# Kernel tuning notes

Measured on AMD Instinct MI355X. Metric: run time of the kernel, lower is better.

## Reference

```python
import jax, jax.numpy as jnp
import numpy as np

B, D_IN = 8192, 4096
H1, H2, LAT = 2048, 1024, 256
NQ, NL = 16, 2


def setup_inputs() -> dict:
    key = jax.random.key(0)
    ks = jax.random.split(key, 16)
    def lin(k, fan_in, fan_out):
        k1, k2 = jax.random.split(k)
        s = 1.0 / np.sqrt(fan_in)
        W = jax.random.uniform(k1, (fan_out, fan_in), jnp.float32, -s, s)
        b = jax.random.uniform(k2, (fan_out,), jnp.float32, -s, s)
        return W, b
    x = jax.random.normal(ks[0], (B, D_IN), jnp.float32)
    We1, be1 = lin(ks[1], D_IN, H1)
    We2, be2 = lin(ks[2], H1, H2)
    We3, be3 = lin(ks[3], H2, LAT)
    P = jax.random.normal(ks[4], (NL, NQ, 3), jnp.float32)  # ansatz params (rx,ry,rz)
    Wd1, bd1 = lin(ks[5], NQ, H2)
    Wd2, bd2 = lin(ks[6], H2, H1)
    Wd3, bd3 = lin(ks[7], H1, D_IN)
    return {"x": x, "We1": We1, "be1": be1, "We2": We2, "be2": be2,
            "We3": We3, "be3": be3, "P": P, "Wd1": Wd1, "bd1": bd1,
            "Wd2": Wd2, "bd2": bd2, "Wd3": Wd3, "bd3": bd3}


def _quantum_block(latent, P):
    """Exact simulation of the per-qubit circuit (all gates single-qubit, so the
    2^n statevector factorizes into per-qubit 2-vectors (a,b) over |0>,|1>).
    latent: (B, LAT), P: (NL, NQ, 3). Returns Z-expectations (B, NQ)."""
    nq = P.shape[1]
    th = latent[:, :nq]  # encoding RY angles, (B, NQ)
    # RY(th)|0> = cos(th/2)|0> + sin(th/2)|1>
    a = jnp.cos(th / 2).astype(jnp.complex64)  # (B, NQ)
    b = jnp.sin(th / 2).astype(jnp.complex64)
    for l in range(P.shape[0]):
        # RX
        t = P[l, :, 0] / 2
        c, s = jnp.cos(t).astype(jnp.complex64), jnp.sin(t).astype(jnp.complex64)
        a, b = c * a - 1j * s * b, -1j * s * a + c * b
        # RY
        t = P[l, :, 1] / 2
        c, s = jnp.cos(t).astype(jnp.complex64), jnp.sin(t).astype(jnp.complex64)
        a, b = c * a - s * b, s * a + c * b
        # RZ
        t = P[l, :, 2] / 2
        ph = jnp.exp(-1j * t.astype(jnp.complex64))
        a, b = a * ph, b * jnp.conj(ph)
    z = (a.real ** 2 + a.imag ** 2) - (b.real ** 2 + b.imag ** 2)
    return z.astype(latent.dtype)


def reference(x, We1, be1, We2, be2, We3, be3, P,
              Wd1, bd1, Wd2, bd2, Wd3, bd3):
    h = jax.nn.relu(x @ We1.T + be1)
    h = jax.nn.relu(h @ We2.T + be2)
    latent = h @ We3.T + be3            # (B, LAT)
    refined = _quantum_block(latent, P)  # (B, NQ)
    h = jax.nn.relu(refined @ Wd1.T + bd1)
    h = jax.nn.relu(h @ Wd2.T + bd2)
    return h @ Wd3.T + bd3              # (B, D_IN)
```

## Files before the change

kernel.cpp:

```cpp
#include <hip/hip_runtime.h>

typedef __attribute__((ext_vector_type(8))) short bf16x8;
typedef __attribute__((ext_vector_type(4))) float f32x4;

__device__ __forceinline__ unsigned short f2bf(float f) {
    union { float f; unsigned int u; } v; v.f = f;
    unsigned int u = v.u;
    unsigned int r = (u + 0x7FFFu + ((u >> 16) & 1u)) >> 16;
    return (unsigned short)r;
}
__device__ __forceinline__ float bf2f(unsigned short b) {
    union { unsigned int u; float f; } v; v.u = ((unsigned int)b) << 16;
    return v.f;
}

#define GL16(g, l)                                                             \
    __builtin_amdgcn_global_load_lds(                                          \
        (__attribute__((address_space(1))) void*)(void*)(g),                   \
        (__attribute__((address_space(3))) void*)(void*)(l), 16, 0, 0)

#define SBAR() __builtin_amdgcn_sched_barrier(0)
#define BAR()  do { SBAR(); __builtin_amdgcn_s_barrier(); SBAR(); } while (0)

struct Cast5 {
    const float *s0, *s1, *s2, *s3, *s4;
    unsigned short *d0, *d1, *d2, *d3, *d4;
    int n0, n1, n2, n3, total;
};
__global__ void castall(Cast5 a) {
    int stride = gridDim.x * blockDim.x;
    for (int i = blockIdx.x * blockDim.x + threadIdx.x; i < a.total; i += stride) {
        int j = i; const float* s; unsigned short* d;
        if (j < a.n0) { s = a.s0; d = a.d0; }
        else { j -= a.n0;
            if (j < a.n1) { s = a.s1; d = a.d1; }
            else { j -= a.n1;
                if (j < a.n2) { s = a.s2; d = a.d2; }
                else { j -= a.n2;
                    if (j < a.n3) { s = a.s3; d = a.d3; }
                    else { j -= a.n3; s = a.s4; d = a.d4; } } } }
        float4 v = ((const float4*)s)[j];
        ushort4 o;
        o.x = f2bf(v.x); o.y = f2bf(v.y); o.z = f2bf(v.z); o.w = f2bf(v.w);
        ((ushort4*)d)[j] = o;
    }
}


template<int RELU, int OUT_BF16, int MP>
__global__ __launch_bounds__(512, 2) void gemm8p(
    const unsigned short* __restrict__ A,
    const unsigned short* __restrict__ Bm,
    const float* __restrict__ bias,
    void* __restrict__ Cout,
    int N, int K, int NT)
{
    constexpr int AHU  = MP * 2048;
    constexpr int BOFF = MP * 8192;
    __shared__ __align__(16) unsigned short lds[MP * 8192 + 32768];

    const int tid  = threadIdx.x;
    const int lane = tid & 63;
    const int w    = tid >> 6;
    const int wm   = w >> 2;
    const int wn   = w & 3;
    const int bm   = blockIdx.y;
    const int bn   = blockIdx.x;

    const long arow0 = (long)bm * (MP * 64);
    const long brow0 = (long)bn * 256;

    const int sc0 = tid,      sc1 = 512 + tid;
    const int sr0 = sc0 >> 3, sr1 = sc1 >> 3;
    const int so0 = (((sc0 & 7) * 16) ^ ((sr0 & 7) << 4)) >> 1;
    const int so1 = (((sc1 & 7) * 16) ^ ((sr1 & 7) << 4)) >> 1;
    const int soff0 = sr0 * K + so0;
    const int soff1 = sr1 * K + so1;
    const int lb0 = (w * 64) * 8;
    const int lb1 = (512 + w * 64) * 8;

    const int cl  = lane & 15;
    const int g16 = (lane >> 4) * 16;
    const int sw  = (cl & 7) << 4;
    const int cK0 = (g16 ^ sw) >> 1;
    const int cK1 = ((64 + g16) ^ sw) >> 1;
    const int arb = wm * (MP * 16) + cl;
    const int brb = wn * 32 + cl;

    f32x4  acc[2][2][MP][2] = {};
    bf16x8 a0[MP][2], a1[MP][2], b0[2][2], b1[2][2];

#define STAGE_A(t2, h) do {                                                    \
        int b_  = (t2) & 1;                                                    \
        int tt_ = (t2) >= NT ? (t2) - NT : (t2);                               \
        const unsigned short* gb_ = A + (arow0 + (long)(h) * (MP * 32)) * (long)K + (long)tt_ * 64; \
        unsigned short* lh_ = &lds[(b_ * 2 + (h)) * AHU];                      \
        GL16(gb_ + soff0, lh_ + lb0);                                          \
        if constexpr (MP == 4) { GL16(gb_ + soff1, lh_ + lb1); }               \
    } while (0)
#define STAGE_B(t2, h) do {                                                    \
        int b_  = (t2) & 1;                                                    \
        int tt_ = (t2) >= NT ? (t2) - NT : (t2);                               \
        const unsigned short* gb_ = Bm + (brow0 + (long)(h) * 128) * (long)K + (long)tt_ * 64; \
        unsigned short* lh_ = &lds[BOFF + (b_ * 2 + (h)) * 8192];              \
        GL16(gb_ + soff0, lh_ + lb0);                                          \
        GL16(gb_ + soff1, lh_ + lb1);                                          \
    } while (0)

#define READA(AR, mh, b_) do {                                                 \
        const unsigned short* ab_ = &lds[((b_) * 2 + (mh)) * AHU];             \
        _Pragma("unroll") for (int mp_ = 0; mp_ < MP; ++mp_) {                 \
            const unsigned short* rp_ = ab_ + (arb + mp_ * 16) * 64;           \
            AR[mp_][0] = *(const bf16x8*)(rp_ + cK0);                          \
            AR[mp_][1] = *(const bf16x8*)(rp_ + cK1);                          \
        }                                                                      \
    } while (0)
#define READB(BR, nh, b_) do {                                                 \
        const unsigned short* bb_ = &lds[BOFF + ((b_) * 2 + (nh)) * 8192];     \
        _Pragma("unroll") for (int np_ = 0; np_ < 2; ++np_) {                  \
            const unsigned short* rp_ = bb_ + (brb + np_ * 16) * 64;           \
            BR[np_][0] = *(const bf16x8*)(rp_ + cK0);                          \
            BR[np_][1] = *(const bf16x8*)(rp_ + cK1);                          \
        }                                                                      \
    } while (0)
#define QUAD(mh, nh, AR, BR) do {                                              \
        __builtin_amdgcn_s_setprio(1);                                         \
        _Pragma("unroll") for (int kk_ = 0; kk_ < 2; ++kk_)                    \
        _Pragma("unroll") for (int mp_ = 0; mp_ < MP; ++mp_)                   \
        _Pragma("unroll") for (int np_ = 0; np_ < 2; ++np_)                    \
            acc[mh][nh][mp_][np_] = __builtin_amdgcn_mfma_f32_16x16x32_bf16(   \
                AR[mp_][kk_], BR[np_][kk_], acc[mh][nh][mp_][np_], 0, 0, 0);   \
        __builtin_amdgcn_s_setprio(0);                                         \
    } while (0)
#define VMW() do {                                                             \
        SBAR();                                                                \
        if constexpr (MP == 4) asm volatile("s_waitcnt vmcnt(6)" ::: "memory");\
        else                   asm volatile("s_waitcnt vmcnt(5)" ::: "memory");\
        SBAR();                                                                \
    } while (0)

    STAGE_B(0, 0); STAGE_A(0, 0); STAGE_B(0, 1); STAGE_A(0, 1);
    STAGE_B(1, 0); STAGE_A(1, 0); STAGE_B(1, 1);
    VMW();
    BAR();
    READA(a0, 0, 0);
    READB(b0, 0, 0);

    for (int t = 0; t < NT; ++t) {
        const int b = t & 1;
        READA(a1, 1, b);
        STAGE_A(t + 1, 1);
        BAR();
        QUAD(0, 0, a0, b0);
        BAR();
        READB(b1, 1, b);
        STAGE_B(t + 2, 0);
        VMW();
        BAR();
        QUAD(0, 1, a0, b1);
        BAR();
        READA(a0, 0, b ^ 1);
        STAGE_A(t + 2, 0);
        BAR();
        QUAD(1, 1, a1, b1);
        BAR();
        STAGE_B(t + 2, 1);
        VMW();
        BAR();
        QUAD(1, 0, a1, b0);
        READB(b0, 0, b ^ 1);
        BAR();
    }

    SBAR(); asm volatile("s_waitcnt vmcnt(0)" ::: "memory"); SBAR();
    BAR();

    const int r4 = (lane >> 4) * 4;
    float bv[2][2];
    #pragma unroll
    for (int nh = 0; nh < 2; ++nh)
        #pragma unroll
        for (int np = 0; np < 2; ++np)
            bv[nh][np] = bias[(long)bn * 256 + nh * 128 + wn * 32 + np * 16 + cl];

    if (OUT_BF16) {
        unsigned short* epi = lds;
        #pragma unroll
        for (int h = 0; h < 2; ++h) {
            if (h) BAR();
            #pragma unroll
            for (int mp = 0; mp < MP; ++mp)
                #pragma unroll
                for (int nh = 0; nh < 2; ++nh)
                    #pragma unroll
                    for (int np = 0; np < 2; ++np)
                        #pragma unroll
                        for (int r = 0; r < 4; ++r) {
                            float v = acc[h][nh][mp][np][r] + bv[nh][np];
                            if (RELU) v = fmaxf(v, 0.f);
                            int lrow = wm * (MP * 16) + mp * 16 + r4 + r;
                            int lcol = nh * 128 + wn * 32 + np * 16 + cl;
                            epi[lrow * 264 + lcol] = f2bf(v);
                        }
            BAR();
            long rowg0 = (long)bm * (MP * 64) + h * (MP * 32);
            #pragma unroll
            for (int i = 0; i < 2 * MP; ++i) {
                int row = (tid >> 5) + i * 16;
                int cc  = (tid & 31) * 8;
                bf16x8 v8 = *(const bf16x8*)&epi[row * 264 + cc];
                *(bf16x8*)((unsigned short*)Cout + (rowg0 + row) * (long)N + (long)bn * 256 + cc) = v8;
            }
        }
    } else {
        #pragma unroll
        for (int mh = 0; mh < 2; ++mh)
            #pragma unroll
            for (int mp = 0; mp < MP; ++mp) {
                long grow = (long)bm * (MP * 64) + mh * (MP * 32) + wm * (MP * 16) + mp * 16 + r4;
                #pragma unroll
                for (int nh = 0; nh < 2; ++nh)
                    #pragma unroll
                    for (int np = 0; np < 2; ++np) {
                        long gcol = (long)bn * 256 + nh * 128 + wn * 32 + np * 16 + cl;
                        #pragma unroll
                        for (int r = 0; r < 4; ++r) {
                            float v = acc[mh][nh][mp][np][r] + bv[nh][np];
                            if (RELU) v = fmaxf(v, 0.f);
                            ((float*)Cout)[(grow + r) * (long)N + gcol] = v;
                        }
                    }
            }
    }
#undef STAGE_A
#undef STAGE_B
#undef READA
#undef READB
#undef QUAD
#undef VMW
}

__global__ __launch_bounds__(256) void latq_d1(
    const unsigned short* __restrict__ h2,
    const float* __restrict__ We3,
    const float* __restrict__ be3,
    const float* __restrict__ P,
    const float* __restrict__ Wd1,
    const float* __restrict__ bd1,
    unsigned short* __restrict__ h3)
{
    __shared__ float zsh[4][16];
    const int lane = threadIdx.x & 63;
    const int wv   = threadIdx.x >> 6;
    const long row = (long)blockIdx.x * 4 + wv;

    float hreg[16];
    const unsigned short* hr = h2 + row * 1024;
    #pragma unroll
    for (int j = 0; j < 16; ++j) hreg[j] = bf2f(hr[lane + 64 * j]);

    float myth = 0.f;
    #pragma unroll
    for (int q = 0; q < 16; ++q) {
        const float* wq = We3 + q * 1024;
        float p = 0.f;
        #pragma unroll
        for (int j = 0; j < 16; ++j) p += hreg[j] * wq[lane + 64 * j];
        #pragma unroll
        for (int o = 32; o; o >>= 1) p += __shfl_xor(p, o, 64);
        if (lane == q) myth = p + be3[q];
    }

    if (lane < 16) {
        const int q = lane;
        float ar = cosf(0.5f * myth), ai = 0.f;
        float br = sinf(0.5f * myth), bi = 0.f;
        #pragma unroll
        for (int l = 0; l < 2; ++l) {
            const float* pp = P + (l * 16 + q) * 3;
            float t, c, s, ar2, ai2, br2, bi2;
            t = 0.5f * pp[0]; c = cosf(t); s = sinf(t);
            ar2 = c * ar + s * bi;  ai2 = c * ai - s * br;
            br2 = c * br + s * ai;  bi2 = c * bi - s * ar;
            ar = ar2; ai = ai2; br = br2; bi = bi2;
            t = 0.5f * pp[1]; c = cosf(t); s = sinf(t);
            ar2 = c * ar - s * br;  ai2 = c * ai - s * bi;
            br2 = s * ar + c * br;  bi2 = s * ai + c * bi;
            ar = ar2; ai = ai2; br = br2; bi = bi2;
            t = 0.5f * pp[2]; c = cosf(t); s = sinf(t);
            ar2 = ar * c + ai * s;  ai2 = ai * c - ar * s;
            br2 = br * c - bi * s;  bi2 = bi * c + br * s;
            ar = ar2; ai = ai2; br = br2; bi = bi2;
        }
        zsh[wv][q] = ar * ar + ai * ai - (br * br + bi * bi);
    }
    __syncthreads();

    float z[16];
    #pragma unroll
    for (int q = 0; q < 16; ++q) z[q] = zsh[wv][q];

    unsigned short* orow = h3 + row * 1024;
    #pragma unroll
    for (int i = 0; i < 16; ++i) {
        int j = lane + 64 * i;
        const float4* wrow = (const float4*)(Wd1 + j * 16);
        float acc = bd1[j];
        #pragma unroll
        for (int qq = 0; qq < 4; ++qq) {
            float4 w4 = wrow[qq];
            acc += z[qq * 4 + 0] * w4.x + z[qq * 4 + 1] * w4.y
                 + z[qq * 4 + 2] * w4.z + z[qq * 4 + 3] * w4.w;
        }
        orow[j] = f2bf(fmaxf(acc, 0.f));
    }
}

extern "C" void kernel_launch(void* const* d_in, const int* in_sizes, int n_in,
                              void* d_out, int out_size, void* d_ws, size_t ws_size,
                              hipStream_t stream) {
    const float* x   = (const float*)d_in[0];
    const float* We1 = (const float*)d_in[1];
    const float* be1 = (const float*)d_in[2];
    const float* We2 = (const float*)d_in[3];
    const float* be2 = (const float*)d_in[4];
    const float* We3 = (const float*)d_in[5];
    const float* be3 = (const float*)d_in[6];
    const float* P   = (const float*)d_in[7];
    const float* Wd1 = (const float*)d_in[8];
    const float* bd1 = (const float*)d_in[9];
    const float* Wd2 = (const float*)d_in[10];
    const float* bd2 = (const float*)d_in[11];
    const float* Wd3 = (const float*)d_in[12];
    const float* bd3 = (const float*)d_in[13];

    const int B = 8192, DIN = 4096, NH1 = 2048, NH2 = 1024;

    char* w = (char*)d_ws;
    unsigned short* x_bf   = (unsigned short*)(w);
    unsigned short* h4     = x_bf;
    unsigned short* We1_bf = (unsigned short*)(w + 67108864L);
    unsigned short* We2_bf = (unsigned short*)(w + 83886080L);
    unsigned short* Wd2_bf = (unsigned short*)(w + 88080384L);
    unsigned short* Wd3_bf = (unsigned short*)(w + 92274688L);
    unsigned short* h1     = (unsigned short*)(w + 109051904L);
    unsigned short* h3     = h1;
    unsigned short* h2     = (unsigned short*)(w + 142606336L);

    Cast5 ca;
    ca.s0 = x;   ca.d0 = x_bf;   ca.n0 = (int)((long)B * DIN / 4);
    ca.s1 = We1; ca.d1 = We1_bf; ca.n1 = (int)((long)NH1 * DIN / 4);
    ca.s2 = We2; ca.d2 = We2_bf; ca.n2 = (int)((long)NH2 * NH1 / 4);
    ca.s3 = Wd2; ca.d3 = Wd2_bf; ca.n3 = (int)((long)NH1 * NH2 / 4);
    ca.s4 = Wd3; ca.d4 = Wd3_bf;
    ca.total = ca.n0 + ca.n1 + ca.n2 + ca.n3 + (int)((long)DIN * NH1 / 4);
    castall<<<2048, 256, 0, stream>>>(ca);

    gemm8p<1, 1, 4><<<dim3(NH1 / 256, B / 256), 512, 0, stream>>>(x_bf, We1_bf, be1, h1, NH1, DIN, DIN >> 6);
    gemm8p<1, 1, 2><<<dim3(NH2 / 256, B / 128), 512, 0, stream>>>(h1, We2_bf, be2, h2, NH2, NH1, NH1 >> 6);
    latq_d1<<<dim3(B / 4), 256, 0, stream>>>(h2, We3, be3, P, Wd1, bd1, h3);
    gemm8p<1, 1, 4><<<dim3(NH1 / 256, B / 256), 512, 0, stream>>>(h3, Wd2_bf, bd2, h4, NH1, NH2, NH2 >> 6);
    gemm8p<0, 0, 4><<<dim3(DIN / 256, B / 256), 512, 0, stream>>>(h4, Wd3_bf, bd3, d_out, DIN, NH1, NH1 >> 6);
}
```

Baseline: 417.4 us.

## Unroll GEMM k-loop by two with pointer-bumped staging and fewer barriers

Unrolls the main bf16 MFMA GEMM loop by two so the LDS buffer parity is a compile-time constant. Global staging addresses become running pointers that are bumped each tile, and LDS read offsets become precomputed byte indices, which removes per-iteration 64-bit address math and modulo logic. It also drops the barrier that followed each MFMA quad, cutting barriers per k-tile from eight to four. The risks are LDS read/write hazards from the removed barriers, and the loop now assumes an even tile count. Past the end it re-fetches the last tile instead of wrapping to the start.

After: 388.6 us. -6.9%, faster.

```diff
diff --git a/kernel.cpp b/kernel.cpp
--- a/kernel.cpp
+++ b/kernel.cpp
@@ -67,15 +67,13 @@
     const int bm   = blockIdx.y;
     const int bn   = blockIdx.x;
 
-    const long arow0 = (long)bm * (MP * 64);
-    const long brow0 = (long)bn * 256;
-
-    const int sc0 = tid,      sc1 = 512 + tid;
-    const int sr0 = sc0 >> 3, sr1 = sc1 >> 3;
-    const int so0 = (((sc0 & 7) * 16) ^ ((sr0 & 7) << 4)) >> 1;
-    const int so1 = (((sc1 & 7) * 16) ^ ((sr1 & 7) << 4)) >> 1;
-    const int soff0 = sr0 * K + so0;
-    const int soff1 = sr1 * K + so1;
+    const unsigned short* gA = A  + (long)bm * (MP * 64) * K;
+    const unsigned short* gB = Bm + (long)bn * 256 * K;
+
+    const int sr0 = tid >> 3;
+    const int so0 = (((tid & 7) * 16) ^ ((sr0 & 7) << 4)) >> 1;
+    const int loff = (sr0 * K + so0) * 2;
+    const int ch1  = K * 128;
     const int lb0 = (w * 64) * 8;
     const int lb1 = (512 + w * 64) * 8;
 
@@ -86,43 +84,38 @@
     const int cK1 = ((64 + g16) ^ sw) >> 1;
     const int arb = wm * (MP * 16) + cl;
     const int brb = wn * 32 + cl;
+    const int aIdx0 = (arb * 64 + cK0) * 2;
+    const int aIdx1 = (arb * 64 + cK1) * 2;
+    const int bIdx0 = (BOFF + brb * 64 + cK0) * 2;
+    const int bIdx1 = (BOFF + brb * 64 + cK1) * 2;
 
     f32x4  acc[2][2][MP][2] = {};
     bf16x8 a0[MP][2], a1[MP][2], b0[2][2], b1[2][2];
 
-#define STAGE_A(t2, h) do {                                                    \
-        int b_  = (t2) & 1;                                                    \
-        int tt_ = (t2) >= NT ? (t2) - NT : (t2);                               \
-        const unsigned short* gb_ = A + (arow0 + (long)(h) * (MP * 32)) * (long)K + (long)tt_ * 64; \
-        unsigned short* lh_ = &lds[(b_ * 2 + (h)) * AHU];                      \
-        GL16(gb_ + soff0, lh_ + lb0);                                          \
-        if constexpr (MP == 4) { GL16(gb_ + soff1, lh_ + lb1); }               \
-    } while (0)
-#define STAGE_B(t2, h) do {                                                    \
-        int b_  = (t2) & 1;                                                    \
-        int tt_ = (t2) >= NT ? (t2) - NT : (t2);                               \
-        const unsigned short* gb_ = Bm + (brow0 + (long)(h) * 128) * (long)K + (long)tt_ * 64; \
-        unsigned short* lh_ = &lds[BOFF + (b_ * 2 + (h)) * 8192];              \
-        GL16(gb_ + soff0, lh_ + lb0);                                          \
-        GL16(gb_ + soff1, lh_ + lb1);                                          \
-    } while (0)
-
-#define READA(AR, mh, b_) do {                                                 \
-        const unsigned short* ab_ = &lds[((b_) * 2 + (mh)) * AHU];             \
+#define GLA_(SP, DI) do {                                                      \
+        GL16((const char*)(SP) + loff, &lds[0] + (DI) + lb0);                  \
+        if constexpr (MP == 4) {                                               \
+            GL16((const char*)(SP) + loff + ch1, &lds[0] + (DI) + lb1); }      \
+    } while (0)
+#define GLB_(SP, DI) do {                                                      \
+        GL16((const char*)(SP) + loff, &lds[0] + (DI) + lb0);                  \
+        GL16((const char*)(SP) + loff + ch1, &lds[0] + (DI) + lb1);            \
+    } while (0)
+
+#define READA_(AR, MH, PAR) do {                                               \
         _Pragma("unroll") for (int mp_ = 0; mp_ < MP; ++mp_) {                 \
-            const unsigned short* rp_ = ab_ + (arb + mp_ * 16) * 64;           \
-            AR[mp_][0] = *(const bf16x8*)(rp_ + cK0);                          \
-            AR[mp_][1] = *(const bf16x8*)(rp_ + cK1);                          \
-        }                                                                      \
-    } while (0)
-#define READB(BR, nh, b_) do {                                                 \
-        const unsigned short* bb_ = &lds[BOFF + ((b_) * 2 + (nh)) * 8192];     \
+            AR[mp_][0] = *(const bf16x8*)((const char*)lds + aIdx0 +           \
+                         (((PAR)*2+(MH))*AHU*2 + mp_*2048));                   \
+            AR[mp_][1] = *(const bf16x8*)((const char*)lds + aIdx1 +           \
+                         (((PAR)*2+(MH))*AHU*2 + mp_*2048));                   \
+        } } while (0)
+#define READB_(BR, NH, PAR) do {                                               \
         _Pragma("unroll") for (int np_ = 0; np_ < 2; ++np_) {                  \
-            const unsigned short* rp_ = bb_ + (brb + np_ * 16) * 64;           \
-            BR[np_][0] = *(const bf16x8*)(rp_ + cK0);                          \
-            BR[np_][1] = *(const bf16x8*)(rp_ + cK1);                          \
-        }                                                                      \
-    } while (0)
+            BR[np_][0] = *(const bf16x8*)((const char*)lds + bIdx0 +           \
+                         (((PAR)*2+(NH))*16384 + np_*2048));                   \
+            BR[np_][1] = *(const bf16x8*)((const char*)lds + bIdx1 +           \
+                         (((PAR)*2+(NH))*16384 + np_*2048));                   \
+        } } while (0)
 #define QUAD(mh, nh, AR, BR) do {                                              \
         __builtin_amdgcn_s_setprio(1);                                         \
         _Pragma("unroll") for (int kk_ = 0; kk_ < 2; ++kk_)                    \
@@ -139,37 +132,53 @@
         SBAR();                                                                \
     } while (0)
 
-    STAGE_B(0, 0); STAGE_A(0, 0); STAGE_B(0, 1); STAGE_A(0, 1);
-    STAGE_B(1, 0); STAGE_A(1, 0); STAGE_B(1, 1);
+    GLB_(gB,                      BOFF + 0);
+    GLA_(gA,                      0);
+    GLB_(gB + (long)128 * K,      BOFF + 8192);
+    GLA_(gA + (long)(MP*32) * K,  AHU);
+    GLB_(gB + 64,                 BOFF + 2*8192);
+    GLA_(gA + 64,                 2*AHU);
+    GLB_(gB + (long)128 * K + 64, BOFF + 3*8192);
     VMW();
     BAR();
-    READA(a0, 0, 0);
-    READB(b0, 0, 0);
-
-    for (int t = 0; t < NT; ++t) {
-        const int b = t & 1;
-        READA(a1, 1, b);
-        STAGE_A(t + 1, 1);
-        BAR();
-        QUAD(0, 0, a0, b0);
-        BAR();
-        READB(b1, 1, b);
-        STAGE_B(t + 2, 0);
-        VMW();
-        BAR();
-        QUAD(0, 1, a0, b1);
-        BAR();
-        READA(a0, 0, b ^ 1);
-        STAGE_A(t + 2, 0);
-        BAR();
-        QUAD(1, 1, a1, b1);
-        BAR();
-        STAGE_B(t + 2, 1);
-        VMW();
-        BAR();
-        QUAD(1, 0, a1, b0);
-        READB(b0, 0, b ^ 1);
-        BAR();
+    READA_(a0, 0, 0);
+    READB_(b0, 0, 0);
+
+    const unsigned short* sA1 = gA + (long)(MP*32) * K + 64;
+    const unsigned short* sA0 = gA + 128;
+    const unsigned short* sB0 = gB + 128;
+    const unsigned short* sB1 = gB + (long)128 * K + 128;
+
+#define KTILE(T, PAR) do {                                                     \
+        const int adv1_ = ((T) + 2 < NT) ? 64 : 0;                             \
+        const int adv2_ = ((T) + 3 < NT) ? 64 : 0;                             \
+                                                                       \
+        READA_(a1, 1, PAR);                                                    \
+        GLA_(sA1, (((PAR)^1)*2+1)*AHU); sA1 += adv1_;                          \
+        BAR();                                                                 \
+        QUAD(0, 0, a0, b0);                                                    \
+                                                                       \
+        READB_(b1, 1, PAR);                                                    \
+        GLB_(sB0, BOFF + (PAR)*2*8192); sB0 += adv2_;                          \
+        VMW();                                                                 \
+        BAR();                                                                 \
+        QUAD(0, 1, a0, b1);                                                    \
+                                                                       \
+        READA_(a0, 0, (PAR)^1);                                                \
+        GLA_(sA0, (PAR)*2*AHU); sA0 += adv2_;                                  \
+        BAR();                                                                 \
+        QUAD(1, 1, a1, b1);                                                    \
+                                                                       \
+        GLB_(sB1, BOFF + ((PAR)*2+1)*8192); sB1 += adv2_;                      \
+        VMW();                                                                 \
+        BAR();                                                                 \
+        QUAD(1, 0, a1, b0);                                                    \
+        READB_(b0, 0, (PAR)^1);                                                \
+    } while (0)
+
+    for (int t = 0; t < NT; t += 2) {
+        KTILE(t, 0);
+        KTILE(t + 1, 1);
     }
 
     SBAR(); asm volatile("s_waitcnt vmcnt(0)" ::: "memory"); SBAR();
@@ -232,12 +241,13 @@
                     }
             }
     }
-#undef STAGE_A
-#undef STAGE_B
-#undef READA
-#undef READB
+#undef GLA_
+#undef GLB_
+#undef READA_
+#undef READB_
 #undef QUAD
 #undef VMW
+#undef KTILE
 }
 
 __global__ __launch_bounds__(256) void latq_d1(
```
